# Performance work log

Measured on AMD Instinct MI355X. Metric: run time of the kernel, lower is better.

The kernel has to match this reference:

```python
import jax, jax.numpy as jnp
import numpy as np
import math

B, LS, G, KNN, DIM, PE, H, DH = 2, 2048, 32, 16, 256, 32, 8, 32
INNER = H * DH
FF = 4 * DIM
EPS = 1e-5


def _ln(x, g, b):
    m = jnp.mean(x, -1, keepdims=True)
    v = jnp.var(x, -1, keepdims=True)
    return (x - m) / jnp.sqrt(v + EPS) * g + b


def _ff(x, w1, b1, w2, b2):
    return jax.nn.gelu(x @ w1 + b1) @ w2 + b2


def setup_inputs():
    key = jax.random.key(0)
    ks = jax.random.split(key, 20)
    def w(i, shape):
        return jax.random.normal(ks[i], shape, jnp.float32) * 0.02
    return {
        'latents': jax.random.normal(ks[0], (B, LS + G, DIM), jnp.float32),
        'topk_indices': jax.random.randint(ks[1], (B, LS, KNN), 0, LS),
        'rpe': jax.random.normal(ks[2], (B, LS, KNN, PE), jnp.float32),
        'self_rpe': jax.random.normal(ks[3], (B, LS, 1, PE), jnp.float32),
        'distances': jax.random.uniform(ks[4], (B, LS, KNN), jnp.float32) * 10.0,
        'num_spatial': LS,
        'sa_wq': w(5, (DIM, INNER)), 'sa_wk': w(6, (DIM + PE, INNER)),
        'sa_wv': w(7, (DIM + PE, INNER)), 'sa_wo': w(8, (INNER, DIM)),
        'sa_bo': jnp.zeros((DIM,)),
        'sa_log_sigma': jnp.full((H,), math.log(3.0), jnp.float32),
        'sa_gbias': jnp.asarray(0.0, jnp.float32),
        'ln1_g': jnp.ones((DIM,)), 'ln1_b': jnp.zeros((DIM,)),
        'ln2_g': jnp.ones((DIM,)), 'ln2_b': jnp.zeros((DIM,)),
        'sff_w1': w(9, (DIM, FF)), 'sff_b1': jnp.zeros((FF,)),
        'sff_w2': w(10, (FF, DIM)), 'sff_b2': jnp.zeros((DIM,)),
        'ga_wq': w(11, (DIM, INNER)), 'ga_wk': w(12, (DIM, INNER)),
        'ga_wv': w(13, (DIM, INNER)), 'ga_wo': w(14, (INNER, DIM)),
        'ga_bo': jnp.zeros((DIM,)),
        'ga_gbias': jnp.asarray(0.0, jnp.float32),
        'ln3_g': jnp.ones((DIM,)), 'ln3_b': jnp.zeros((DIM,)),
        'ln4_g': jnp.ones((DIM,)), 'ln4_b': jnp.zeros((DIM,)),
        'gff_w1': w(15, (DIM, FF)), 'gff_b1': jnp.zeros((FF,)),
        'gff_w2': w(16, (FF, DIM)), 'gff_b2': jnp.zeros((DIM,)),
    }


def _forward(latents, topk_indices, rpe, self_rpe, distances, num_spatial, p):
    L = num_spatial
    spatial = latents[:, :L]
    glob = latents[:, L:]
    b, _, d = spatial.shape
    g = glob.shape[1]
    scale = DH ** -0.5
    # ---- spatial local attention: context = [self, kNN neighbors, all globals] ----
    x = _ln(spatial, p['ln1_g'], p['ln1_b'])
    neighbors = jax.vmap(lambda s, idx: s[idx])(x, topk_indices)  # [B,L,k,D] gather
    glob_exp = jnp.broadcast_to(glob[:, None], (b, L, g, d))
    ctx = jnp.concatenate([x[:, :, None, :], neighbors, glob_exp], axis=2)  # [B,L,1+k+G,D]
    rpe_cat = jnp.concatenate([self_rpe, rpe, jnp.zeros((b, L, g, PE), x.dtype)], axis=2)
    ctx = jnp.concatenate([ctx, rpe_cat], axis=-1)  # [B,L,C,D+PE]
    q = (x @ p['sa_wq']).reshape(b, L, H, DH)
    kk = (ctx @ p['sa_wk']).reshape(b, L, -1, H, DH)
    vv = (ctx @ p['sa_wv']).reshape(b, L, -1, H, DH)
    attn = jnp.einsum('blhd,blchd->bhlc', q, kk) * scale
    sigma_sq = jnp.exp(2.0 * p['sa_log_sigma'])  # [H]
    dist_sp = jnp.concatenate([jnp.zeros((b, L, 1), x.dtype), distances], axis=2)  # [B,L,1+k]
    gauss = -(dist_sp ** 2)[:, None] / (2.0 * sigma_sq[None, :, None, None])  # [B,H,L,1+k]
    bias = jnp.concatenate([gauss, jnp.broadcast_to(p['sa_gbias'], (b, H, L, g))], axis=-1)
    attn = jax.nn.softmax(attn + bias, axis=-1)
    out = jnp.einsum('bhlc,blchd->blhd', attn, vv).reshape(b, L, INNER)
    spatial = spatial + out @ p['sa_wo'] + p['sa_bo']
    spatial = spatial + _ff(_ln(spatial, p['ln2_g'], p['ln2_b']), p['sff_w1'], p['sff_b1'], p['sff_w2'], p['sff_b2'])
    # ---- global full attention: Q=global, K/V=[updated spatial; normed global] ----
    gq_in = _ln(glob, p['ln3_g'], p['ln3_b'])
    kv = jnp.concatenate([spatial, gq_in], axis=1)  # [B,L+G,D]
    qg = (gq_in @ p['ga_wq']).reshape(b, g, H, DH)
    kg = (kv @ p['ga_wk']).reshape(b, L + g, H, DH)
    vg = (kv @ p['ga_wv']).reshape(b, L + g, H, DH)
    a2 = jnp.einsum('bghd,bchd->bhgc', qg, kg) * scale + p['ga_gbias']
    a2 = jax.nn.softmax(a2, axis=-1)
    og = jnp.einsum('bhgc,bchd->bghd', a2, vg).reshape(b, g, INNER)
    glob = glob + og @ p['ga_wo'] + p['ga_bo']
    glob = glob + _ff(_ln(glob, p['ln4_g'], p['ln4_b']), p['gff_w1'], p['gff_b1'], p['gff_w2'], p['gff_b2'])
    return jnp.concatenate([spatial, glob], axis=1)


def reference(latents, topk_indices, rpe, self_rpe, distances, num_spatial,
              sa_wq, sa_wk, sa_wv, sa_wo, sa_bo, sa_log_sigma, sa_gbias,
              ln1_g, ln1_b, ln2_g, ln2_b, sff_w1, sff_b1, sff_w2, sff_b2,
              ga_wq, ga_wk, ga_wv, ga_wo, ga_bo, ga_gbias,
              ln3_g, ln3_b, ln4_g, ln4_b, gff_w1, gff_b1, gff_w2, gff_b2):
    p = dict(sa_wq=sa_wq, sa_wk=sa_wk, sa_wv=sa_wv, sa_wo=sa_wo, sa_bo=sa_bo,
             sa_log_sigma=sa_log_sigma, sa_gbias=sa_gbias,
             ln1_g=ln1_g, ln1_b=ln1_b, ln2_g=ln2_g, ln2_b=ln2_b,
             sff_w1=sff_w1, sff_b1=sff_b1, sff_w2=sff_w2, sff_b2=sff_b2,
             ga_wq=ga_wq, ga_wk=ga_wk, ga_wv=ga_wv, ga_wo=ga_wo, ga_bo=ga_bo,
             ga_gbias=ga_gbias, ln3_g=ln3_g, ln3_b=ln3_b, ln4_g=ln4_g, ln4_b=ln4_b,
             gff_w1=gff_w1, gff_b1=gff_b1, gff_w2=gff_w2, gff_b2=gff_b2)
    return _forward(latents, topk_indices, rpe, self_rpe, distances, num_spatial, p)
```

## Files before the change

### kernel.cpp

```cpp
#include <hip/hip_runtime.h>
#include <math.h>

#define LS 2048
#define NG 32
#define ROWS_B 2080
#define DIM 256
#define PE 32
#define NH 8
#define DH 32
#define NCTX 49
#define SCALE 0.17677669529663687f
#define QSTR 1536

typedef __attribute__((ext_vector_type(8))) short short8;
typedef __attribute__((ext_vector_type(4))) float f32x4;
typedef __attribute__((ext_vector_type(4))) unsigned short us4;

__device__ __forceinline__ unsigned short f2bf(float x)
{
    unsigned int u = __float_as_uint(x);
    unsigned int r = (u + 0x7fffu + ((u >> 16) & 1u)) >> 16;
    return (unsigned short)r;
}
__device__ __forceinline__ float bf2f(unsigned short v)
{
    return __uint_as_float((unsigned int)v << 16);
}
__device__ __forceinline__ float4 bf2f4(us4 v)
{
    return (float4){ bf2f(v.x), bf2f(v.y), bf2f(v.z), bf2f(v.w) };
}
__device__ __forceinline__ float dot4(float4 a, float4 b)
{
    return a.x * b.x + a.y * b.y + a.z * b.z + a.w * b.w;
}
__device__ __forceinline__ float gelu_f(float x)
{
    float x3 = x * x * x;
    return 0.5f * x * (1.0f + tanhf(0.7978845608028654f * (x + 0.044715f * x3)));
}

struct WEnt { const float* src; unsigned short* dst; int K; int N; int t0; };
struct WTab { WEnt e[9]; };

__global__ __launch_bounds__(256) void wprep_k(
    WTab tab,
    const float* __restrict__ sa_wq, const float* __restrict__ sa_wk,
    const float* __restrict__ sa_wv, const float* __restrict__ sa_wo,
    unsigned short* __restrict__ wt_qkvw, unsigned short* __restrict__ wt_wo2,
    const float* __restrict__ latents,
    const float* __restrict__ g1, const float* __restrict__ b1,
    const float* __restrict__ g3, const float* __restrict__ b3,
    unsigned short* __restrict__ Xb, float* __restrict__ GQ)
{
    __shared__ unsigned short tile[64][72];
    __shared__ float red[8];
    int blk = blockIdx.x, t = threadIdx.x;
    if (blk < 512) {
        const float* wkpe = sa_wk + 256 * 256;
        const float* wvpe = sa_wv + 256 * 256;
        if (blk < 256) {
            int j = blk, h = j >> 5, p = j & 31;
            const float* wq = sa_wq + (size_t)t * 256 + h * 32;
            const float* wk = wkpe + (size_t)p * 256 + h * 32;
            float acc = 0.0f;
            #pragma unroll
            for (int dd = 0; dd < 32; ++dd) acc += wq[dd] * wk[dd];
            wt_qkvw[(size_t)(768 + j) * 256 + t] = f2bf(acc);
        } else {
            int n = blk - 256;
            #pragma unroll
            for (int kk = 0; kk < 2; ++kk) {
                int k = t + kk * 256;
                float v;
                if (k < 256) v = sa_wo[(size_t)k * 256 + n];
                else {
                    int j = k - 256, h = j >> 5, p = j & 31;
                    float a = 0.0f;
                    #pragma unroll
                    for (int dd = 0; dd < 32; ++dd)
                        a += wvpe[(size_t)p * 256 + h * 32 + dd] * sa_wo[(size_t)(h * 32 + dd) * 256 + n];
                    v = a;
                }
                wt_wo2[(size_t)n * 512 + k] = f2bf(v);
            }
        }
    } else if (blk < 736) {
        int local0 = blk - 512;
        int i = 0;
        #pragma unroll
        for (int j = 1; j < 9; ++j) if (local0 >= tab.e[j].t0) i = j;
        const float* W = tab.e[i].src;
        unsigned short* Wt = tab.e[i].dst;
        int K = tab.e[i].K, N = tab.e[i].N;
        int local = local0 - tab.e[i].t0;
        int nb = N >> 6;
        int n0 = (local % nb) * 64, k0 = (local / nb) * 64;
        #pragma unroll
        for (int r = 0; r < 4; ++r) {
            int k = r * 16 + (t >> 4);
            int n = (t & 15) * 4;
            float4 wv = *(const float4*)(W + (size_t)(k0 + k) * N + n0 + n);
            tile[k][n + 0] = f2bf(wv.x);
            tile[k][n + 1] = f2bf(wv.y);
            tile[k][n + 2] = f2bf(wv.z);
            tile[k][n + 3] = f2bf(wv.w);
        }
        __syncthreads();
        #pragma unroll
        for (int r = 0; r < 4; ++r) {
            int n = r * 16 + (t >> 4);
            int k = (t & 15) * 4;
            us4 o;
            o.x = tile[k + 0][n];
            o.y = tile[k + 1][n];
            o.z = tile[k + 2][n];
            o.w = tile[k + 3][n];
            *(us4*)(Wt + (size_t)(n0 + n) * K + k0 + k) = o;
        }
    } else {
        int blk2 = blk - 736;
        const float* gam; const float* bet; size_t ip;
        if (blk2 < 4096) {
            int b = blk2 >> 11;
            ip = ((size_t)b * ROWS_B + (blk2 & 2047)) * DIM + t;
            gam = g1; bet = b1;
        } else {
            int r2 = blk2 - 4096;
            int b = r2 >> 5;
            ip = ((size_t)b * ROWS_B + LS + (r2 & 31)) * DIM + t;
            gam = g3; bet = b3;
        }
        float v = latents[ip];
        float a = v, b2 = v * v;
        #pragma unroll
        for (int m = 32; m >= 1; m >>= 1) { a += __shfl_xor(a, m); b2 += __shfl_xor(b2, m); }
        if ((t & 63) == 0) { red[t >> 6] = a; red[4 + (t >> 6)] = b2; }
        __syncthreads();
        float mean = (red[0] + red[1] + red[2] + red[3]) * (1.0f / 256.0f);
        float var  = (red[4] + red[5] + red[6] + red[7]) * (1.0f / 256.0f) - mean * mean;
        float y = (v - mean) * rsqrtf(var + 1e-5f) * gam[t] + bet[t];
        if (blk2 < 4096) Xb[(size_t)blk2 * DIM + t] = f2bf(y);
        else             GQ[(size_t)(blk2 - 4096) * DIM + t] = y;
    }
}

__global__ __launch_bounds__(256) void ln_rows_k(
    const float* __restrict__ in, const float* __restrict__ gam,
    const float* __restrict__ bet, unsigned short* __restrict__ out)
{
    __shared__ float red[8];
    int r = blockIdx.x, t = threadIdx.x;
    int b = r >> 11;
    size_t ip = ((size_t)b * ROWS_B + (r & 2047)) * DIM + t;
    float v = in[ip];
    float a = v, b2 = v * v;
    #pragma unroll
    for (int m = 32; m >= 1; m >>= 1) { a += __shfl_xor(a, m); b2 += __shfl_xor(b2, m); }
    if ((t & 63) == 0) { red[t >> 6] = a; red[4 + (t >> 6)] = b2; }
    __syncthreads();
    float mean = (red[0] + red[1] + red[2] + red[3]) * (1.0f / 256.0f);
    float var  = (red[4] + red[5] + red[6] + red[7]) * (1.0f / 256.0f) - mean * mean;
    out[(size_t)r * DIM + t] = f2bf((v - mean) * rsqrtf(var + 1e-5f) * gam[t] + bet[t]);
}

__global__ __launch_bounds__(256) void wgs_k(
    const unsigned short* __restrict__ wtq, const unsigned short* __restrict__ kvglb,
    unsigned short* __restrict__ wgs)
{
    int n = blockIdx.x, k = threadIdx.x;
    int h = n & 7, cg = n >> 3;
    float acc = 0.0f;
    #pragma unroll
    for (int dd = 0; dd < 32; ++dd)
        acc += bf2f(wtq[(size_t)(h * 32 + dd) * 256 + k]) * bf2f(kvglb[(size_t)cg * 512 + h * 32 + dd]);
    wgs[(size_t)n * 256 + k] = f2bf(acc);
}

template<int BIAS, int DOGELU, int RES, int ABF16, int CBF16>
__device__ __forceinline__ void mgemm_body(
    const void* __restrict__ Av, const unsigned short* __restrict__ Bt,
    const float* __restrict__ bias, const float* __restrict__ Res,
    void* __restrict__ Cv, int N, int K, int bstr,
    int arpb, int absr, int aoff, int crpb, int cbsr, int coff,
    int col0, int row0)
{
    __shared__ unsigned short Asl[64][64];
    __shared__ unsigned short Bsl[64][64];
    int t = threadIdx.x;
    int lane = t & 63, w = t >> 6;
    int wr = w >> 1, wc = w & 1;
    int lrow = lane & 15, lk = lane >> 4;

    int srow = t >> 4;
    int scol = (t & 15) << 2;
    int sslot = (t & 15) >> 1;
    int shalf = (t & 15) & 1;

    f32x4 acc[2][2];
    #pragma unroll
    for (int m = 0; m < 2; ++m)
        #pragma unroll
        for (int n = 0; n < 2; ++n)
            acc[m][n] = (f32x4){0.f, 0.f, 0.f, 0.f};

    for (int kk = 0; kk < K; kk += 64) {
        #pragma unroll
        for (int r = 0; r < 4; ++r) {
            int row = r * 16 + srow;
            int ar = row0 + row;
            size_t ab = ((size_t)(ar / arpb) * absr + aoff + (ar % arpb)) * (size_t)K + kk + scol;
            us4 ap;
            if (ABF16) {
                ap = *(const us4*)((const unsigned short*)Av + ab);
            } else {
                float4 av = *(const float4*)((const float*)Av + ab);
                ap.x = f2bf(av.x); ap.y = f2bf(av.y); ap.z = f2bf(av.z); ap.w = f2bf(av.w);
            }
            *(us4*)&Asl[row][((sslot ^ (row & 7)) << 3) + (shalf << 2)] = ap;
            us4 bv = *(const us4*)(Bt + (size_t)(col0 + row) * bstr + kk + scol);
            *(us4*)&Bsl[row][((sslot ^ (row & 7)) << 3) + (shalf << 2)] = bv;
        }
        __syncthreads();
        #pragma unroll
        for (int k2 = 0; k2 < 2; ++k2) {
            short8 af[2], bfr[2];
            #pragma unroll
            for (int m = 0; m < 2; ++m) {
                int rowA = wr * 32 + m * 16 + lrow;
                af[m] = *(short8*)&Asl[rowA][((k2 * 4 + lk) ^ (rowA & 7)) << 3];
                int rowB = wc * 32 + m * 16 + lrow;
                bfr[m] = *(short8*)&Bsl[rowB][((k2 * 4 + lk) ^ (rowB & 7)) << 3];
            }
            #pragma unroll
            for (int m = 0; m < 2; ++m)
                #pragma unroll
                for (int n = 0; n < 2; ++n)
                    acc[m][n] = __builtin_amdgcn_mfma_f32_16x16x32_bf16(af[m], bfr[n], acc[m][n], 0, 0, 0);
        }
        __syncthreads();
    }
    #pragma unroll
    for (int m = 0; m < 2; ++m) {
        #pragma unroll
        for (int n = 0; n < 2; ++n) {
            int col = col0 + wc * 32 + n * 16 + lrow;
            #pragma unroll
            for (int j = 0; j < 4; ++j) {
                int r = row0 + wr * 32 + m * 16 + lk * 4 + j;
                size_t cp = ((size_t)(r / crpb) * cbsr + coff + (r % crpb)) * (size_t)N + col;
                float o = acc[m][n][j];
                if (BIAS)   o += bias[col];
                if (DOGELU) o = gelu_f(o);
                if (RES)    o += Res[cp];
                if (CBF16) ((unsigned short*)Cv)[cp] = f2bf(o);
                else       ((float*)Cv)[cp] = o;
            }
        }
    }
}

template<int BIAS, int DOGELU, int RES, int ABF16, int CBF16>
__global__ __launch_bounds__(256) void mgemm_k(
    const void* __restrict__ Av, const unsigned short* __restrict__ Bt,
    const float* __restrict__ bias, const float* __restrict__ Res,
    void* __restrict__ Cv, int M, int N, int K, int bstr,
    int arpb, int absr, int aoff, int crpb, int cbsr, int coff)
{
    mgemm_body<BIAS, DOGELU, RES, ABF16, CBF16>(
        Av, Bt, bias, Res, Cv, N, K, bstr, arpb, absr, aoff, crpb, cbsr, coff,
        blockIdx.x * 64, blockIdx.y * 64);
}

__global__ __launch_bounds__(256) void kvg_pair_k(
    const float* __restrict__ outp, const float* __restrict__ GQ,
    const unsigned short* __restrict__ wt_gakv,
    unsigned short* __restrict__ KVGb, unsigned short* __restrict__ GKVQb)
{
    int x = blockIdx.x, y = blockIdx.y;
    if (x < 8) {
        mgemm_body<0,0,0,0,1>(outp, wt_gakv, nullptr, nullptr, KVGb,
            512, 256, 256, LS, ROWS_B, 0, 4096, 4096, 0, x * 64, y * 64);
    } else {
        if (y != 0) return;
        mgemm_body<0,0,0,0,1>(GQ, wt_gakv, nullptr, nullptr, GKVQb,
            768, 256, 256, 64, 64, 0, 64, 64, 0, (x - 8) * 64, 0);
    }
}

__global__ __launch_bounds__(256) void attn_sp_k(
    const unsigned short* __restrict__ QKV, const unsigned short* __restrict__ KVGLb,
    const int* __restrict__ idx, const float* __restrict__ rpe,
    const float* __restrict__ srpe, const float* __restrict__ dist,
    const float* __restrict__ lsig, const float* __restrict__ gbias,
    unsigned short* __restrict__ ORb)
{
    __shared__ float s_rpe[17 * 32];
    __shared__ float s_sc[NCTX * 8];
    __shared__ float s_red[32 * 64];
    __shared__ float s_d[16];
    __shared__ int   s_row[17];
    int t = threadIdx.x;
    int r = blockIdx.x;
    int b = r >> 11;
    int w = t >> 6, lane = t & 63;
    int h = lane >> 3, dg = lane & 7;

    if (t < 32) s_rpe[t] = srpe[(size_t)r * 32 + t];
    for (int i = t; i < 512; i += 256) s_rpe[32 + i] = rpe[(size_t)r * 512 + i];
    if (t < 16) {
        s_row[t + 1] = (b << 11) + idx[r * 16 + t];
        s_d[t] = dist[(size_t)r * 16 + t];
    }
    if (t == 16) s_row[0] = r;

    size_t qb = (size_t)r * QSTR + lane * 4;
    float4 q4  = bf2f4(*(const us4*)(QKV + qb));
    float4 qw4 = bf2f4(*(const us4*)(QKV + qb + 768));
    float inv2s = 1.0f / (2.0f * __expf(2.0f * lsig[h]));
    float gb = gbias[0];
    __syncthreads();

    us4 kreg[5], vreg[5];
    #pragma unroll
    for (int i = 0; i < 5; ++i) {
        int c = w + 4 * i;
        if (c < 17) {
            const unsigned short* rowp = QKV + (size_t)s_row[c] * QSTR + lane * 4;
            kreg[i] = *(const us4*)(rowp + 256);
            vreg[i] = *(const us4*)(rowp + 512);
        }
    }
    float sc_loc[5];
    #pragma unroll
    for (int i = 0; i < 5; ++i) {
        int c = w + 4 * i;
        if (c < 17) {
            float4 k4 = bf2f4(kreg[i]);
            float4 rv4 = *(const float4*)&s_rpe[c * 32 + dg * 4];
            float part = dot4(q4, k4) + dot4(rv4, qw4);
            part += __shfl_xor(part, 1);
            part += __shfl_xor(part, 2);
            part += __shfl_xor(part, 4);
            float bia = (c == 0) ? 0.0f : -s_d[c - 1] * s_d[c - 1] * inv2s;
            float sval = part * SCALE + bia;
            if (dg == 0) s_sc[c * 8 + h] = sval;
            sc_loc[i] = sval;
        }
    }
    float sc_glob[8];
    #pragma unroll
    for (int i = 0; i < 8; ++i) {
        int gi = w + 4 * i;
        float sval = bf2f(QKV[(size_t)r * QSTR + 1024 + (((size_t)b * 32 + gi) << 3) + h]) * SCALE + gb;
        if (dg == 0) s_sc[(17 + gi) * 8 + h] = sval;
        sc_glob[i] = sval;
    }
    __syncthreads();

    float vals[7];
    float lm = -3.0e38f;
    #pragma unroll
    for (int i = 0; i < 7; ++i) {
        int cc = dg + 8 * i;
        if (cc < NCTX) { float v = s_sc[cc * 8 + h]; vals[i] = v; lm = fmaxf(lm, v); }
    }
    lm = fmaxf(lm, __shfl_xor(lm, 1));
    lm = fmaxf(lm, __shfl_xor(lm, 2));
    lm = fmaxf(lm, __shfl_xor(lm, 4));
    float ls = 0.0f;
    #pragma unroll
    for (int i = 0; i < 7; ++i) {
        int cc = dg + 8 * i;
        if (cc < NCTX) ls += __expf(vals[i] - lm);
    }
    ls += __shfl_xor(ls, 1);
    ls += __shfl_xor(ls, 2);
    ls += __shfl_xor(ls, 4);
    float inv = 1.0f / ls;

    float4 acc4 = (float4){0, 0, 0, 0}, racc4 = (float4){0, 0, 0, 0};
    #pragma unroll
    for (int i = 0; i < 5; ++i) {
        int c = w + 4 * i;
        if (c < 17) {
            float p = __expf(sc_loc[i] - lm);
            float4 v4 = bf2f4(vreg[i]);
            float4 rv4 = *(const float4*)&s_rpe[c * 32 + dg * 4];
            racc4.x += p * rv4.x; racc4.y += p * rv4.y;
            racc4.z += p * rv4.z; racc4.w += p * rv4.w;
            acc4.x += p * v4.x; acc4.y += p * v4.y;
            acc4.z += p * v4.z; acc4.w += p * v4.w;
        }
    }
    #pragma unroll
    for (int i = 0; i < 8; ++i) {
        int gi = w + 4 * i;
        float p = __expf(sc_glob[i] - lm);
        float4 v4 = bf2f4(*(const us4*)(KVGLb + ((size_t)(b * NG + gi)) * 512 + 256 + lane * 4));
        acc4.x += p * v4.x; acc4.y += p * v4.y;
        acc4.z += p * v4.z; acc4.w += p * v4.w;
    }

    s_red[(w * 8 + 0) * 64 + lane] = acc4.x;
    s_red[(w * 8 + 1) * 64 + lane] = acc4.y;
    s_red[(w * 8 + 2) * 64 + lane] = acc4.z;
    s_red[(w * 8 + 3) * 64 + lane] = acc4.w;
    s_red[(w * 8 + 4) * 64 + lane] = racc4.x;
    s_red[(w * 8 + 5) * 64 + lane] = racc4.y;
    s_red[(w * 8 + 6) * 64 + lane] = racc4.z;
    s_red[(w * 8 + 7) * 64 + lane] = racc4.w;
    __syncthreads();
    {
        int j = w;
        float a = 0.0f, rr = 0.0f;
        #pragma unroll
        for (int ww = 0; ww < 4; ++ww) {
            a  += s_red[(ww * 8 + j) * 64 + lane];
            rr += s_red[(ww * 8 + 4 + j) * 64 + lane];
        }
        int e = h * 32 + dg * 4 + j;
        ORb[(size_t)r * 512 + e]       = f2bf(a * inv);
        ORb[(size_t)r * 512 + 256 + e] = f2bf(rr * inv);
    }
}

__global__ __launch_bounds__(256) void ga_scores_k(
    const unsigned short* __restrict__ GKVQ, const unsigned short* __restrict__ KVG,
    float* __restrict__ A2)
{
    int t = threadIdx.x;
    int bh = blockIdx.x;
    int b = bh >> 3, h = bh & 7;
    int w = t >> 6, lane = t & 63;
    int ct = blockIdx.y * 4 + w;
    if (ct >= 130) return;
    int lr = lane & 15, lq = lane >> 4;

    short8 aq0 = *(const short8*)(GKVQ + ((size_t)(b * 32 + lr)) * 768 + 512 + h * 32 + lq * 8);
    short8 aq1 = *(const short8*)(GKVQ + ((size_t)(b * 32 + 16 + lr)) * 768 + 512 + h * 32 + lq * 8);
    int c = ct * 16 + lr;
    const unsigned short* kr = (c < LS)
        ? KVG + ((size_t)(b * LS + c)) * 512 + h * 32 + lq * 8
        : GKVQ + ((size_t)(b * NG + (c - LS))) * 768 + h * 32 + lq * 8;
    short8 bk = *(const short8*)kr;

    f32x4 acc0 = (f32x4){0, 0, 0, 0}, acc1 = (f32x4){0, 0, 0, 0};
    acc0 = __builtin_amdgcn_mfma_f32_16x16x32_bf16(aq0, bk, acc0, 0, 0, 0);
    acc1 = __builtin_amdgcn_mfma_f32_16x16x32_bf16(aq1, bk, acc1, 0, 0, 0);

    float* arow = A2 + ((size_t)(b * NH + h) * NG) * ROWS_B + ct * 16 + lr;
    #pragma unroll
    for (int j = 0; j < 4; ++j) {
        arow[(size_t)(lq * 4 + j) * ROWS_B]        = acc0[j] * SCALE;
        arow[(size_t)(16 + lq * 4 + j) * ROWS_B]   = acc1[j] * SCALE;
    }
}

__global__ __launch_bounds__(256) void ga_softmax_k(float* __restrict__ A2, float* __restrict__ rinv)
{
    __shared__ float red[8];
    int t = threadIdx.x;
    float* row = A2 + (size_t)blockIdx.x * ROWS_B;
    float lm = -1e30f;
    for (int i = t; i < ROWS_B; i += 256) lm = fmaxf(lm, row[i]);
    #pragma unroll
    for (int m = 32; m >= 1; m >>= 1) lm = fmaxf(lm, __shfl_xor(lm, m));
    if ((t & 63) == 0) red[t >> 6] = lm;
    __syncthreads();
    float M = fmaxf(fmaxf(red[0], red[1]), fmaxf(red[2], red[3]));
    float ls = 0.0f;
    for (int i = t; i < ROWS_B; i += 256) {
        float e = __expf(row[i] - M);
        row[i] = e;
        ls += e;
    }
    #pragma unroll
    for (int m = 32; m >= 1; m >>= 1) ls += __shfl_xor(ls, m);
    if ((t & 63) == 0) red[4 + (t >> 6)] = ls;
    __syncthreads();
    if (t == 0) rinv[blockIdx.x] = 1.0f / (red[4] + red[5] + red[6] + red[7]);
}

__global__ __launch_bounds__(256) void ga_wv_k(
    const float* __restrict__ A2, const float* __restrict__ rinv,
    const unsigned short* __restrict__ GKVQ,
    const unsigned short* __restrict__ KVG, float* __restrict__ OGP)
{
    __shared__ float s_acc[8][256];
    int t = threadIdx.x;
    int bg = blockIdx.x;
    int s = blockIdx.y;
    int b = bg >> 5, g = bg & 31;
    int tt = t & 31, sub = t >> 5;
    int h = tt >> 2;
    const float* w = A2 + ((size_t)(b * NH + h) * NG + g) * ROWS_B;
    int c0 = s * 65, cend = c0 + 65;
    float acc[8] = {};
    for (int c = c0 + sub; c < cend; c += 8) {
        float p = w[c];
        const unsigned short* vr = (c < LS)
            ? KVG + ((size_t)(b * LS + c)) * 512 + 256 + tt * 8
            : GKVQ + ((size_t)(b * NG + (c - LS))) * 768 + 256 + tt * 8;
        us4 v0 = *(const us4*)vr;
        us4 v1 = *(const us4*)(vr + 4);
        acc[0] += p * bf2f(v0.x); acc[1] += p * bf2f(v0.y);
        acc[2] += p * bf2f(v0.z); acc[3] += p * bf2f(v0.w);
        acc[4] += p * bf2f(v1.x); acc[5] += p * bf2f(v1.y);
        acc[6] += p * bf2f(v1.z); acc[7] += p * bf2f(v1.w);
    }
    #pragma unroll
    for (int j = 0; j < 8; ++j) s_acc[sub][tt * 8 + j] = acc[j];
    __syncthreads();
    float o = 0.0f;
    #pragma unroll
    for (int ss = 0; ss < 8; ++ss) o += s_acc[ss][t];
    o *= rinv[((size_t)b * NH + (t >> 5)) * NG + g];
    OGP[((size_t)bg * 32 + s) * 256 + t] = o;
}

__global__ __launch_bounds__(1024) void glob_tail_k(
    const float* __restrict__ OGP, const float* __restrict__ latents,
    const float* __restrict__ ga_wo, const float* __restrict__ ga_bo,
    const float* __restrict__ ln4g, const float* __restrict__ ln4b,
    const float* __restrict__ w1, const float* __restrict__ b1,
    const float* __restrict__ w2, const float* __restrict__ b2,
    float* __restrict__ GTP)
{
    __shared__ float s_part[4][256];
    __shared__ float s_og[256];
    __shared__ float s_y[256];
    __shared__ float s_h1[256];
    __shared__ float red[16];
    int bg = blockIdx.x, q = blockIdx.y, t = threadIdx.x;
    int tt = t & 255, grp = t >> 8;

    float og = 0.0f;
    #pragma unroll
    for (int s = 0; s < 8; ++s)
        og += OGP[((size_t)bg * 32 + grp * 8 + s) * 256 + tt];
    s_part[grp][tt] = og;
    __syncthreads();
    if (grp == 0) s_og[tt] = s_part[0][tt] + s_part[1][tt] + s_part[2][tt] + s_part[3][tt];
    __syncthreads();

    float x = 0.0f;
    {
        int k0 = grp * 64;
        #pragma unroll 16
        for (int k = k0; k < k0 + 64; ++k) x += s_og[k] * ga_wo[(size_t)k * 256 + tt];
    }
    s_part[grp][tt] = x;
    __syncthreads();
    int b = bg >> 5;
    size_t row = (size_t)b * ROWS_B + LS + (bg & 31);
    float res = latents[row * 256 + tt]
              + s_part[0][tt] + s_part[1][tt] + s_part[2][tt] + s_part[3][tt] + ga_bo[tt];

    float a = res, b2s = res * res;
    #pragma unroll
    for (int m = 32; m >= 1; m >>= 1) { a += __shfl_xor(a, m); b2s += __shfl_xor(b2s, m); }
    if ((t & 63) == 0 && t < 256) { red[t >> 6] = a; red[8 + (t >> 6)] = b2s; }
    __syncthreads();
    float mean = (red[0] + red[1] + red[2] + red[3]) * (1.0f / 256.0f);
    float var  = (red[8] + red[9] + red[10] + red[11]) * (1.0f / 256.0f) - mean * mean;
    float y = (res - mean) * rsqrtf(var + 1e-5f) * ln4g[tt] + ln4b[tt];
    if (grp == 0) s_y[tt] = y;
    __syncthreads();

    float h1p = 0.0f;
    {
        int k0 = grp * 64;
        #pragma unroll 16
        for (int k = k0; k < k0 + 64; ++k) h1p += s_y[k] * w1[(size_t)k * 1024 + q * 256 + tt];
    }
    s_part[grp][tt] = h1p;
    __syncthreads();
    if (grp == 0)
        s_h1[tt] = gelu_f(b1[q * 256 + tt]
                 + s_part[0][tt] + s_part[1][tt] + s_part[2][tt] + s_part[3][tt]);
    __syncthreads();

    float o = 0.0f;
    {
        int j0 = grp * 64;
        #pragma unroll 16
        for (int j = j0; j < j0 + 64; ++j) o += s_h1[j] * w2[(size_t)(q * 256 + j) * 256 + tt];
    }
    s_part[grp][tt] = o;
    __syncthreads();
    if (grp == 0) {
        float v = s_part[0][tt] + s_part[1][tt] + s_part[2][tt] + s_part[3][tt];
        if (q == 0) v += res + b2[tt];
        GTP[((size_t)bg * 4 + q) * 256 + tt] = v;
    }
}

__global__ __launch_bounds__(256) void glob_fin_k(
    const float* __restrict__ GTP, float* __restrict__ out)
{
    int bg = blockIdx.x, t = threadIdx.x;
    int b = bg >> 5;
    size_t row = (size_t)b * ROWS_B + LS + (bg & 31);
    float v = GTP[((size_t)bg * 4 + 0) * 256 + t] + GTP[((size_t)bg * 4 + 1) * 256 + t]
            + GTP[((size_t)bg * 4 + 2) * 256 + t] + GTP[((size_t)bg * 4 + 3) * 256 + t];
    out[row * 256 + t] = v;
}

extern "C" void kernel_launch(void* const* d_in, const int* in_sizes, int n_in,
                              void* d_out, int out_size, void* d_ws, size_t ws_size,
                              hipStream_t stream)
{
    const float* latents = (const float*)d_in[0];
    const int*   idx     = (const int*)d_in[1];
    const float* rpe     = (const float*)d_in[2];
    const float* srpe    = (const float*)d_in[3];
    const float* dist    = (const float*)d_in[4];
    const float* sa_wq   = (const float*)d_in[6];
    const float* sa_wk   = (const float*)d_in[7];
    const float* sa_wv   = (const float*)d_in[8];
    const float* sa_wo   = (const float*)d_in[9];
    const float* sa_bo   = (const float*)d_in[10];
    const float* lsig    = (const float*)d_in[11];
    const float* gbias   = (const float*)d_in[12];
    const float* ln1g    = (const float*)d_in[13];
    const float* ln1b    = (const float*)d_in[14];
    const float* ln2g    = (const float*)d_in[15];
    const float* ln2b    = (const float*)d_in[16];
    const float* sff_w1  = (const float*)d_in[17];
    const float* sff_b1  = (const float*)d_in[18];
    const float* sff_w2  = (const float*)d_in[19];
    const float* sff_b2  = (const float*)d_in[20];
    const float* ga_wq   = (const float*)d_in[21];
    const float* ga_wk   = (const float*)d_in[22];
    const float* ga_wv   = (const float*)d_in[23];
    const float* ga_wo   = (const float*)d_in[24];
    const float* ga_bo   = (const float*)d_in[25];
    const float* ln3g    = (const float*)d_in[27];
    const float* ln3b    = (const float*)d_in[28];
    const float* ln4g    = (const float*)d_in[29];
    const float* ln4b    = (const float*)d_in[30];
    const float* gff_w1  = (const float*)d_in[31];
    const float* gff_b1  = (const float*)d_in[32];
    const float* gff_w2  = (const float*)d_in[33];
    const float* gff_b2  = (const float*)d_in[34];
    float* out = (float*)d_out;

    const size_t SZ = (size_t)4096 * 256;
    float* ws = (float*)d_ws;
    unsigned short* Xb = (unsigned short*)ws;
    unsigned short* QKV2b = (unsigned short*)(ws + SZ);
    unsigned short* H1b  = QKV2b;
    unsigned short* KVGb = QKV2b;
    unsigned short* ORb  = (unsigned short*)(ws + 4 * SZ);
    float* A2  = ws + 5 * SZ;
    float* OGP = A2 + (size_t)2 * NH * NG * ROWS_B;
    float* GTP = OGP + (size_t)64 * 32 * 256;
    float* RINV = GTP + (size_t)64 * 4 * 256;
    unsigned short* wt = (unsigned short*)(ws + 7 * SZ);
    unsigned short* wt_qkvw = wt;
    unsigned short* wgs_w   = wt + 262144;
    unsigned short* wt_ff1  = wt + 393216;
    unsigned short* wt_ff2  = wt + 655360;
    unsigned short* wt_gakv = wt + 917504;
    unsigned short* wt_wo2  = wt + 1114112;
    float* smalls = ws + 8 * SZ;
    unsigned short* KVGLb = (unsigned short*)smalls;
    float* GQ = smalls + 16384;
    unsigned short* GKVQb = (unsigned short*)(GQ + 16384);

    dim3 blk(256);

    WTab tab;
    tab.e[0] = { sa_wq,  wt_qkvw,           256,  256,   0 };
    tab.e[1] = { sa_wk,  wt_qkvw + 65536,   256,  256,  16 };
    tab.e[2] = { sa_wv,  wt_qkvw + 131072,  256,  256,  32 };
    tab.e[3] = { sff_w1, wt_ff1,            256, 1024,  48 };
    tab.e[4] = { sff_w2, wt_ff2,           1024,  256, 112 };
    tab.e[5] = { ga_wk,  wt_gakv,           256,  256, 176 };
    tab.e[6] = { ga_wv,  wt_gakv + 65536,   256,  256, 192 };
    tab.e[7] = { ga_wq,  wt_gakv + 131072,  256,  256, 208 };
    tab.e[8] = { sa_wq,  wt_qkvw,           256,  256, 1 << 30 };

    wprep_k<<<dim3(4896), blk, 0, stream>>>(tab, sa_wq, sa_wk, sa_wv, sa_wo,
                                            wt_qkvw, wt_wo2, latents,
                                            ln1g, ln1b, ln3g, ln3b, Xb, GQ);

    mgemm_k<0,0,0,0,1><<<dim3(8,1), blk, 0, stream>>>(latents, wt_qkvw + 65536, nullptr, nullptr, KVGLb,
        64,512,256,256, 32,ROWS_B,LS, 64,64,0);
    wgs_k<<<dim3(512), blk, 0, stream>>>(wt_qkvw, KVGLb, wgs_w);

    mgemm_k<0,0,0,1,1><<<dim3(24,64), blk, 0, stream>>>(Xb, wt_qkvw, nullptr, nullptr, QKV2b,
        4096,QSTR,256,256, 4096,4096,0, 4096,4096,0);

    attn_sp_k<<<dim3(4096), blk, 0, stream>>>(QKV2b, KVGLb, idx, rpe, srpe, dist,
                                              lsig, gbias, ORb);

    mgemm_k<1,0,1,1,0><<<dim3(4,64), blk, 0, stream>>>(ORb, wt_wo2, sa_bo, latents, out,
        4096,256,512,512, 4096,4096,0, LS,ROWS_B,0);

    ln_rows_k<<<dim3(4096), blk, 0, stream>>>(out, ln2g, ln2b, Xb);
    mgemm_k<1,1,0,1,1><<<dim3(16,64), blk, 0, stream>>>(Xb, wt_ff1, sff_b1, nullptr, H1b,
        4096,1024,256,256, 4096,4096,0, 4096,4096,0);
    mgemm_k<1,0,1,1,0><<<dim3(4,64), blk, 0, stream>>>(H1b, wt_ff2, sff_b2, out, out,
        4096,256,1024,1024, 4096,4096,0, LS,ROWS_B,0);

    kvg_pair_k<<<dim3(20,64), blk, 0, stream>>>(out, GQ, wt_gakv, KVGb, GKVQb);

    ga_scores_k<<<dim3(16, 33), blk, 0, stream>>>(GKVQb, KVGb, A2);
    ga_softmax_k<<<dim3(512), blk, 0, stream>>>(A2, RINV);
    ga_wv_k<<<dim3(64, 32), blk, 0, stream>>>(A2, RINV, GKVQb, KVGb, OGP);

    glob_tail_k<<<dim3(64, 4), dim3(1024), 0, stream>>>(OGP, latents, ga_wo, ga_bo, ln4g, ln4b,
                                                        gff_w1, gff_b1, gff_w2, gff_b2, GTP);
    glob_fin_k<<<dim3(64), blk, 0, stream>>>(GTP, out);
}
```

Baseline: 137.1 us.

## Fuse LayerNorm into the QKV and FF1 GEMM prologues

```diff
diff --git a/kernel.cpp b/kernel.cpp
--- a/kernel.cpp
+++ b/kernel.cpp
@@ -49,9 +49,8 @@
     const float* __restrict__ sa_wv, const float* __restrict__ sa_wo,
     unsigned short* __restrict__ wt_qkvw, unsigned short* __restrict__ wt_wo2,
     const float* __restrict__ latents,
-    const float* __restrict__ g1, const float* __restrict__ b1,
     const float* __restrict__ g3, const float* __restrict__ b3,
-    unsigned short* __restrict__ Xb, float* __restrict__ GQ)
+    float* __restrict__ GQ)
 {
     __shared__ unsigned short tile[64][72];
     __shared__ float red[8];
@@ -119,18 +118,9 @@
             *(us4*)(Wt + (size_t)(n0 + n) * K + k0 + k) = o;
         }
     } else {
-        int blk2 = blk - 736;
-        const float* gam; const float* bet; size_t ip;
-        if (blk2 < 4096) {
-            int b = blk2 >> 11;
-            ip = ((size_t)b * ROWS_B + (blk2 & 2047)) * DIM + t;
-            gam = g1; bet = b1;
-        } else {
-            int r2 = blk2 - 4096;
-            int b = r2 >> 5;
-            ip = ((size_t)b * ROWS_B + LS + (r2 & 31)) * DIM + t;
-            gam = g3; bet = b3;
-        }
+        int r2 = blk - 736;
+        int b = r2 >> 5;
+        size_t ip = ((size_t)b * ROWS_B + LS + (r2 & 31)) * DIM + t;
         float v = latents[ip];
         float a = v, b2 = v * v;
         #pragma unroll
@@ -139,29 +129,8 @@
         __syncthreads();
         float mean = (red[0] + red[1] + red[2] + red[3]) * (1.0f / 256.0f);
         float var  = (red[4] + red[5] + red[6] + red[7]) * (1.0f / 256.0f) - mean * mean;
-        float y = (v - mean) * rsqrtf(var + 1e-5f) * gam[t] + bet[t];
-        if (blk2 < 4096) Xb[(size_t)blk2 * DIM + t] = f2bf(y);
-        else             GQ[(size_t)(blk2 - 4096) * DIM + t] = y;
-    }
-}
-
-__global__ __launch_bounds__(256) void ln_rows_k(
-    const float* __restrict__ in, const float* __restrict__ gam,
-    const float* __restrict__ bet, unsigned short* __restrict__ out)
-{
-    __shared__ float red[8];
-    int r = blockIdx.x, t = threadIdx.x;
-    int b = r >> 11;
-    size_t ip = ((size_t)b * ROWS_B + (r & 2047)) * DIM + t;
-    float v = in[ip];
-    float a = v, b2 = v * v;
-    #pragma unroll
-    for (int m = 32; m >= 1; m >>= 1) { a += __shfl_xor(a, m); b2 += __shfl_xor(b2, m); }
-    if ((t & 63) == 0) { red[t >> 6] = a; red[4 + (t >> 6)] = b2; }
-    __syncthreads();
-    float mean = (red[0] + red[1] + red[2] + red[3]) * (1.0f / 256.0f);
-    float var  = (red[4] + red[5] + red[6] + red[7]) * (1.0f / 256.0f) - mean * mean;
-    out[(size_t)r * DIM + t] = f2bf((v - mean) * rsqrtf(var + 1e-5f) * gam[t] + bet[t]);
+        GQ[(size_t)r2 * DIM + t] = (v - mean) * rsqrtf(var + 1e-5f) * g3[t] + b3[t];
+    }
 }
 
 __global__ __launch_bounds__(256) void wgs_k(
@@ -270,6 +239,109 @@
     mgemm_body<BIAS, DOGELU, RES, ABF16, CBF16>(
         Av, Bt, bias, Res, Cv, N, K, bstr, arpb, absr, aoff, crpb, cbsr, coff,
         blockIdx.x * 64, blockIdx.y * 64);
+}
+
+template<int BIAS, int DOGELU>
+__global__ __launch_bounds__(256) void lnmm_k(
+    const float* __restrict__ A, const unsigned short* __restrict__ Bt,
+    const float* __restrict__ gam, const float* __restrict__ bet,
+    const float* __restrict__ bias, unsigned short* __restrict__ Cb,
+    int N, int arpb, int absr, int aoff)
+{
+    __shared__ unsigned short Asl[64][64];
+    __shared__ unsigned short Bsl[64][64];
+    __shared__ float s_mean[64];
+    __shared__ float s_rstd[64];
+    int t = threadIdx.x;
+    int col0 = blockIdx.x * 64, row0 = blockIdx.y * 64;
+    int lane = t & 63, w = t >> 6;
+    int wr = w >> 1, wc = w & 1;
+    int lrow = lane & 15, lk = lane >> 4;
+
+    {
+        int sr = t >> 2, part = t & 3;
+        int ar = row0 + sr;
+        const float* rp = A + ((size_t)(ar / arpb) * absr + aoff + (ar % arpb)) * 256 + part * 64;
+        float s1 = 0.0f, s2 = 0.0f;
+        #pragma unroll 16
+        for (int j = 0; j < 64; ++j) { float v = rp[j]; s1 += v; s2 += v * v; }
+        s1 += __shfl_xor(s1, 1); s2 += __shfl_xor(s2, 1);
+        s1 += __shfl_xor(s1, 2); s2 += __shfl_xor(s2, 2);
+        if (part == 0) {
+            float mean = s1 * (1.0f / 256.0f);
+            float var  = s2 * (1.0f / 256.0f) - mean * mean;
+            s_mean[sr] = mean;
+            s_rstd[sr] = rsqrtf(var + 1e-5f);
+        }
+    }
+    __syncthreads();
+
+    int srow = t >> 4;
+    int scol = (t & 15) << 2;
+    int sslot = (t & 15) >> 1;
+    int shalf = (t & 15) & 1;
+
+    f32x4 acc[2][2];
+    #pragma unroll
+    for (int m = 0; m < 2; ++m)
+        #pragma unroll
+        for (int n = 0; n < 2; ++n)
+            acc[m][n] = (f32x4){0.f, 0.f, 0.f, 0.f};
+
+    for (int kk = 0; kk < 256; kk += 64) {
+        float4 g4 = *(const float4*)(gam + kk + scol);
+        float4 b4 = *(const float4*)(bet + kk + scol);
+        #pragma unroll
+        for (int r = 0; r < 4; ++r) {
+            int row = r * 16 + srow;
+            int ar = row0 + row;
+            size_t ab = ((size_t)(ar / arpb) * absr + aoff + (ar % arpb)) * 256 + kk + scol;
+            float4 av = *(const float4*)(A + ab);
+            float mn = s_mean[row], rs = s_rstd[row];
+            us4 ap;
+            ap.x = f2bf((av.x - mn) * rs * g4.x + b4.x);
+            ap.y = f2bf((av.y - mn) * rs * g4.y + b4.y);
+            ap.z = f2bf((av.z - mn) * rs * g4.z + b4.z);
+            ap.w = f2bf((av.w - mn) * rs * g4.w + b4.w);
+            *(us4*)&Asl[row][((sslot ^ (row & 7)) << 3) + (shalf << 2)] = ap;
+            us4 bv = *(const us4*)(Bt + (size_t)(col0 + row) * 256 + kk + scol);
+            *(us4*)&Bsl[row][((sslot ^ (row & 7)) << 3) + (shalf << 2)] = bv;
+        }
+        __syncthreads();
+        #pragma unroll
+        for (int k2 = 0; k2 < 2; ++k2) {
+            short8 af[2], bfr[2];
+            #pragma unroll
+            for (int m = 0; m < 2; ++m) {
+                int rowA = wr * 32 + m * 16 + lrow;
+                af[m] = *(short8*)&Asl[rowA][((k2 * 4 + lk) ^ (rowA & 7)) << 3];
+                int rowB = wc * 32 + m * 16 + lrow;
+                bfr[m] = *(short8*)&Bsl[rowB][((k2 * 4 + lk) ^ (rowB & 7)) << 3];
+            }
+            #pragma unroll
+            for (int m = 0; m < 2; ++m)
+                #pragma unroll
+                for (int n = 0; n < 2; ++n)
+                    acc[m][n] = __builtin_amdgcn_mfma_f32_16x16x32_bf16(af[m], bfr[n], acc[m][n], 0, 0, 0);
+        }
+        __syncthreads();
+    }
+    #pragma unroll
+    for (int m = 0; m < 2; ++m) {
+        #pragma unroll
+        for (int n = 0; n < 2; ++n) {
+            int col = col0 + wc * 32 + n * 16 + lrow;
+            #pragma unroll
+            for (int j = 0; j < 4; ++j) {
+                int r = row0 + wr * 32 + m * 16 + lk * 4 + j;
+                size_t cp = (size_t)r * N + col;
+                float o = acc[m][n][j];
+                if (BIAS)   o += bias[col];
+                if (DOGELU) o = gelu_f(o);
+                Cb[cp] = f2bf(o);
+            }
+        }
+    }
 }
 
 __global__ __launch_bounds__(256) void kvg_pair_k(
@@ -648,7 +720,6 @@
 
     const size_t SZ = (size_t)4096 * 256;
     float* ws = (float*)d_ws;
-    unsigned short* Xb = (unsigned short*)ws;
     unsigned short* QKV2b = (unsigned short*)(ws + SZ);
     unsigned short* H1b  = QKV2b;
     unsigned short* KVGb = QKV2b;
@@ -682,16 +753,16 @@
     tab.e[7] = { ga_wq,  wt_gakv + 131072,  256,  256, 208 };
     tab.e[8] = { sa_wq,  wt_qkvw,           256,  256, 1 << 30 };
 
-    wprep_k<<<dim3(4896), blk, 0, stream>>>(tab, sa_wq, sa_wk, sa_wv, sa_wo,
-                                            wt_qkvw, wt_wo2, latents,
-                                            ln1g, ln1b, ln3g, ln3b, Xb, GQ);
+    wprep_k<<<dim3(800), blk, 0, stream>>>(tab, sa_wq, sa_wk, sa_wv, sa_wo,
+                                           wt_qkvw, wt_wo2, latents,
+                                           ln3g, ln3b, GQ);
 
     mgemm_k<0,0,0,0,1><<<dim3(8,1), blk, 0, stream>>>(latents, wt_qkvw + 65536, nullptr, nullptr, KVGLb,
         64,512,256,256, 32,ROWS_B,LS, 64,64,0);
     wgs_k<<<dim3(512), blk, 0, stream>>>(wt_qkvw, KVGLb, wgs_w);
 
-    mgemm_k<0,0,0,1,1><<<dim3(24,64), blk, 0, stream>>>(Xb, wt_qkvw, nullptr, nullptr, QKV2b,
-        4096,QSTR,256,256, 4096,4096,0, 4096,4096,0);
+    lnmm_k<0,0><<<dim3(24,64), blk, 0, stream>>>(latents, wt_qkvw, ln1g, ln1b, nullptr, QKV2b,
+        QSTR, LS, ROWS_B, 0);
 
     attn_sp_k<<<dim3(4096), blk, 0, stream>>>(QKV2b, KVGLb, idx, rpe, srpe, dist,
                                               lsig, gbias, ORb);
@@ -699,9 +770,8 @@
     mgemm_k<1,0,1,1,0><<<dim3(4,64), blk, 0, stream>>>(ORb, wt_wo2, sa_bo, latents, out,
         4096,256,512,512, 4096,4096,0, LS,ROWS_B,0);
 
-    ln_rows_k<<<dim3(4096), blk, 0, stream>>>(out, ln2g, ln2b, Xb);
-    mgemm_k<1,1,0,1,1><<<dim3(16,64), blk, 0, stream>>>(Xb, wt_ff1, sff_b1, nullptr, H1b,
-        4096,1024,256,256, 4096,4096,0, 4096,4096,0);
+    lnmm_k<1,1><<<dim3(16,64), blk, 0, stream>>>(out, wt_ff1, ln2g, ln2b, sff_b1, H1b,
+        1024, LS, ROWS_B, 0);
     mgemm_k<1,0,1,1,0><<<dim3(4,64), blk, 0, stream>>>(H1b, wt_ff2, sff_b2, out, out,
         4096,256,1024,1024, 4096,4096,0, LS,ROWS_B,0);
 
```

Measured after the change: 153.4 us. 11.9% more time.
